# Optimization experiments

Measured on AMD Instinct MI355X. Metric: run time of the kernel, lower is better.

## Reference

```python
import jax, jax.numpy as jnp
import numpy as np

N_NODES = 100000
N_GRAPHS = 256
N_EDGES = 800000


def gcn_conv(x, W, b, src, dst):
    """PyG GCNConv: self-loops + symmetric deg^-1/2 normalization + scatter-add."""
    h = x @ W  # [N, F_out]
    # degree on graph with self-loops (edge weight 1)
    deg = jax.ops.segment_sum(jnp.ones((src.shape[0],), h.dtype), dst,
                              num_segments=N_NODES) + 1.0
    dinv = jax.lax.rsqrt(deg)  # deg^-1/2, deg >= 1 so finite
    norm = dinv[src] * dinv[dst]  # [E]
    msg = h[src] * norm[:, None]  # gather + scale, [E, F_out]
    agg = jax.ops.segment_sum(msg, dst, num_segments=N_NODES)
    # self-loop contribution: dinv[i]^2 * h[i]
    agg = agg + h * (dinv * dinv)[:, None]
    return agg + b


def setup_inputs() -> dict:
    key = jax.random.key(0)
    ks = jax.random.split(key, 16)
    inp = {
        "x": jax.random.normal(ks[0], (N_NODES, 114), jnp.float32),
        "edge_index": jax.random.randint(ks[1], (2, N_EDGES), 0, N_NODES, jnp.int64)
        if jax.config.jax_enable_x64 else jax.random.randint(ks[1], (2, N_EDGES), 0, N_NODES, jnp.int32),
        "batch": jnp.sort(jax.random.randint(ks[2], (N_NODES,), 0, N_GRAPHS,
                                             jnp.int32)),
        "W1": jax.random.normal(ks[3], (114, 230), jnp.float32) * 0.09,
        "b1": jax.random.normal(ks[4], (230,), jnp.float32) * 0.01,
        "W2": jax.random.normal(ks[5], (230, 115), jnp.float32) * 0.07,
        "b2": jax.random.normal(ks[6], (115,), jnp.float32) * 0.01,
        "Wg": jax.random.normal(ks[7], (115, 64), jnp.float32) * 0.09,
        "bg": jax.random.normal(ks[8], (64,), jnp.float32) * 0.01,
        "Wf": jax.random.normal(ks[9], (64, 32), jnp.float32) * 0.12,
        "bf": jax.random.normal(ks[10], (32,), jnp.float32) * 0.01,
        "Wo": jax.random.normal(ks[11], (32, 1), jnp.float32) * 0.17,
        "bo": jax.random.normal(ks[12], (1,), jnp.float32) * 0.01,
    }
    return inp


def reference(x, edge_index, batch, W1, b1, W2, b2, Wg, bg, Wf, bf, Wo, bo):
    src, dst = edge_index[0], edge_index[1]
    h = jax.nn.relu(gcn_conv(x, W1, b1, src, dst))
    # dropout p=0.2 is identity at inference (training=False)
    h = jax.nn.relu(gcn_conv(h, W2, b2, src, dst))
    # global max pool over graphs; h >= 0 after relu so clamp empty segments to 0
    pooled = jax.ops.segment_max(h, batch, num_segments=N_GRAPHS)
    pooled = jnp.maximum(pooled, 0.0)  # [G, 115]
    g = jax.nn.relu(pooled @ Wg + bg)
    g = jax.nn.relu(g @ Wf + bf)
    return g @ Wo + bo  # [G, 1]
```

## Files before the change

### kernel.cpp

```cpp
#include <hip/hip_runtime.h>
#include <hip/hip_bf16.h>
#include <hip/hip_fp16.h>

#define NN 100000
#define NG 256
#define NE 800000

constexpr int F0 = 114;
constexpr int F1 = 230;
constexpr int F2 = 115;
constexpr int MPAD = 100096;

typedef _Float16 __attribute__((ext_vector_type(8))) f16x8;
typedef __attribute__((ext_vector_type(4))) float f32x4;
typedef __attribute__((ext_vector_type(8))) unsigned short u16x8;

__device__ __forceinline__ unsigned short f2h_bits(float x) {
  _Float16 h = (_Float16)x;
  return __builtin_bit_cast(unsigned short, h);
}
__device__ __forceinline__ float h_bits2f(unsigned short u) {
  return (float)__builtin_bit_cast(_Float16, u);
}

__device__ __forceinline__ void bar_nodrain() {
  asm volatile("s_waitcnt lgkmcnt(0)" ::: "memory");
  __builtin_amdgcn_s_barrier();
}


__global__ void k_count(const int* __restrict__ dst, int* __restrict__ cnt) {
  int e = blockIdx.x * blockDim.x + threadIdx.x;
  if (e < NE) atomicAdd(&cnt[dst[e]], 1);
}

constexpr int SCAN_T = 256;
constexpr int SCAN_E = 1024;
constexpr int NB = (NN + SCAN_E - 1) / SCAN_E;

__global__ void k_scan1(const int* __restrict__ cnt, int* __restrict__ off,
                        int* __restrict__ bsum, float* __restrict__ dinv) {
  __shared__ int s[SCAN_T];
  int b = blockIdx.x, t = threadIdx.x;
  int base = b * SCAN_E + t * 4;
  int v0 = 0, v1 = 0, v2 = 0, v3 = 0;
  if (base + 0 < NN) v0 = cnt[base + 0];
  if (base + 1 < NN) v1 = cnt[base + 1];
  if (base + 2 < NN) v2 = cnt[base + 2];
  if (base + 3 < NN) v3 = cnt[base + 3];
  if (base + 0 < NN) dinv[base + 0] = rsqrtf((float)v0 + 1.0f);
  if (base + 1 < NN) dinv[base + 1] = rsqrtf((float)v1 + 1.0f);
  if (base + 2 < NN) dinv[base + 2] = rsqrtf((float)v2 + 1.0f);
  if (base + 3 < NN) dinv[base + 3] = rsqrtf((float)v3 + 1.0f);
  int sum = v0 + v1 + v2 + v3;
  s[t] = sum;
  __syncthreads();
  for (int ofs = 1; ofs < SCAN_T; ofs <<= 1) {
    int x = (t >= ofs) ? s[t - ofs] : 0;
    __syncthreads();
    s[t] += x;
    __syncthreads();
  }
  int excl = s[t] - sum;
  if (base + 0 < NN) off[base + 0] = excl;
  if (base + 1 < NN) off[base + 1] = excl + v0;
  if (base + 2 < NN) off[base + 2] = excl + v0 + v1;
  if (base + 3 < NN) off[base + 3] = excl + v0 + v1 + v2;
  if (t == SCAN_T - 1) bsum[b] = s[t];
}

__global__ void k_scan3(int* __restrict__ off, const int* __restrict__ bsum,
                        int* __restrict__ cur) {
  __shared__ int pre;
  int b = blockIdx.x, t = threadIdx.x;
  int seg = b >> 2;
  if (t < 64) {
    int s = 0;
    for (int j = t; j < seg; j += 64) s += bsum[j];
#pragma unroll
    for (int o = 1; o < 64; o <<= 1) s += __shfl_xor(s, o);
    if (t == 0) pre = s;
  }
  __syncthreads();
  int i = b * 256 + t;
  if (i < NN) {
    int v = off[i] + pre;
    off[i] = v;
    cur[i] = v;
  }
  if (i == NN) off[NN] = NE;
}


constexpr int FB_PLACE = (NE + 255) / 256;
constexpr int FB_PREPX = NN / 2;
constexpr int FB_PREPB = 256;
constexpr int FB_POOL  = (NG * F2 + 255) / 256;

__global__ __launch_bounds__(256) void k_fatB(
    const int* __restrict__ src, const int* __restrict__ dst,
    int* __restrict__ cur, int* __restrict__ srcs,
    const float* __restrict__ x, const float* __restrict__ dinv,
    unsigned short* __restrict__ xd,
    const float* __restrict__ W1, const float* __restrict__ W2,
    unsigned short* __restrict__ B1, unsigned short* __restrict__ B2,
    float* __restrict__ pooled) {
  int b = blockIdx.x, t = threadIdx.x;
  if (b < FB_PLACE) {
    int e = b * 256 + t;
    if (e < NE) {
      int p = atomicAdd(&cur[dst[e]], 1);
      srcs[p] = src[e];
    }
  } else if (b < FB_PLACE + FB_PREPX) {
    int bb = b - FB_PLACE;
    int n = bb * 2 + (t >> 7);
    int f = t & 127;
    float v = (f < F0) ? x[(size_t)n * F0 + f] * dinv[n] : 0.0f;
    xd[(size_t)n * 128 + f] = f2h_bits(v);
  } else if (b < FB_PLACE + FB_PREPX + FB_PREPB) {
    int bb = b - (FB_PLACE + FB_PREPX);
    if (bb < 128) {
      int n = bb * 2 + (t >> 7), k = t & 127;
      float v = (k < F0 && n < F1) ? W1[(size_t)k * F1 + n] : 0.0f;
      B1[(size_t)n * 128 + k] = f2h_bits(v);
    } else {
      int n = bb - 128, k = t;
      float v = (k < F1 && n < F2) ? W2[(size_t)k * F2 + n] : 0.0f;
      B2[(size_t)n * 256 + k] = f2h_bits(v);
    }
  } else {
    int bb = b - (FB_PLACE + FB_PREPX + FB_PREPB);
    int i = bb * 256 + t;
    if (i < NG * F2) pooled[i] = 0.0f;
  }
}


template <bool POOL>
__global__ __launch_bounds__(256) void k_gatherw(
    const unsigned short* __restrict__ tab, const float* __restrict__ dinv,
    const int* __restrict__ off, const int* __restrict__ srcs,
    const float* __restrict__ b2, const int* __restrict__ batch,
    unsigned short* __restrict__ outh, float* __restrict__ pooled) {
  __shared__ float smax[4][128];
  __shared__ int sg[4];
  int w = threadIdx.x >> 6, lane = threadIdx.x & 63;
  int n = blockIdx.x * 4 + w;
  int grp = lane >> 4, sub = lane & 15;
  int fb = sub * 8;

  float acc[8] = {0.f, 0.f, 0.f, 0.f, 0.f, 0.f, 0.f, 0.f};
  int j0 = off[n], j1 = off[n + 1];
  for (int base = j0; base <= j1; base += 16) {
    int row[4];
    u16x8 v[4];
    bool has[4];
#pragma unroll
    for (int c = 0; c < 4; ++c) {
      int je = base + c * 4 + grp;
      row[c] = (je < j1) ? srcs[je] : ((je == j1) ? n : -1);
      has[c] = row[c] >= 0;
    }
#pragma unroll
    for (int c = 0; c < 4; ++c)
      if (has[c]) v[c] = *(const u16x8*)&tab[(size_t)row[c] * 128 + fb];
#pragma unroll
    for (int c = 0; c < 4; ++c)
      if (has[c]) {
#pragma unroll
        for (int u = 0; u < 8; ++u) acc[u] += h_bits2f(v[c][u]);
      }
  }
#pragma unroll
  for (int u = 0; u < 8; ++u) {
    acc[u] += __shfl_xor(acc[u], 16);
    acc[u] += __shfl_xor(acc[u], 32);
  }
  float dn = dinv[n];

  if constexpr (!POOL) {
    if (grp == 0) {
      u16x8 o;
#pragma unroll
      for (int u = 0; u < 8; ++u) o[u] = f2h_bits(acc[u] * dn);
      *(u16x8*)&outh[(size_t)n * 128 + fb] = o;
    }
  } else {
    if (grp == 0) {
#pragma unroll
      for (int u = 0; u < 8; ++u) {
        int f = fb + u;
        float bb = (f < F2) ? b2[f] : 0.0f;
        smax[w][f] = fmaxf(acc[u] * dn + bb, 0.0f);
      }
      if (sub == 0) sg[w] = batch[n];
    }
    __syncthreads();
    int t = threadIdx.x;
    if (t < 128) {
      int g0 = sg[0];
      bool same = (sg[1] == g0) & (sg[2] == g0) & (sg[3] == g0);
      if (same) {
        float m = fmaxf(fmaxf(smax[0][t], smax[1][t]),
                        fmaxf(smax[2][t], smax[3][t]));
        if (t < F2 && m > 0.0f)
          atomicMax((int*)&pooled[g0 * F2 + t], __float_as_int(m));
      } else {
        for (int ww = 0; ww < 4; ++ww) {
          float m = smax[ww][t];
          if (t < F2 && m > 0.0f)
            atomicMax((int*)&pooled[sg[ww] * F2 + t], __float_as_int(m));
        }
      }
    }
  }
}


__global__ __launch_bounds__(256, 3) void k_fused(
    const unsigned short* __restrict__ A,
    const unsigned short* __restrict__ B1,
    const unsigned short* __restrict__ B2,
    const float* __restrict__ b1, const float* __restrict__ dscale,
    unsigned short* __restrict__ td) {
  __shared__ char lds[49152];
  char* AsB = lds;
  char* h1B = lds + 16384;
  char* Bs  = lds + 32768;

  const int t = threadIdx.x;
  const int m0 = blockIdx.x * 64;
  const int lane = t & 63, w = t >> 6;
  const int r = lane & 15;
  const int kq = lane >> 4;
  const int kb16 = kq * 16;
  const int rq = kq * 4;
  const int wc = w * 32;
  const int swr = (r & 7) << 4;
  const int arow = t >> 2, aseg = t & 3, aswz = (arow & 7) << 4;
  const int brow = t >> 1, bseg = t & 1, bswz = (brow & 7) << 4;

  {
    size_t ga = (size_t)(m0 + arow) * 128 + aseg * 32;
#pragma unroll
    for (int v = 0; v < 4; ++v) {
      u16x8 d = *(const u16x8*)&A[ga + v * 8];
      *(u16x8*)(AsB + arow * 256 + ((aseg * 64 + v * 16) ^ aswz)) = d;
    }
  }
  u16x8 ph[4];
  {
    size_t gb = (size_t)brow * 128 + bseg * 32;
#pragma unroll
    for (int v = 0; v < 4; ++v) ph[v] = *(const u16x8*)&B1[gb + v * 8];
  }

  f32x4 acc1[4][2], acc2[4][2];
#pragma unroll
  for (int i = 0; i < 4; ++i)
#pragma unroll
    for (int j = 0; j < 2; ++j) {
      acc1[i][j] = (f32x4){0.f, 0.f, 0.f, 0.f};
      acc2[i][j] = (f32x4){0.f, 0.f, 0.f, 0.f};
    }

#pragma unroll
  for (int rd = 0; rd < 8; ++rd) {
    const int h = rd >> 2, phase = (rd >> 1) & 1, kc = rd & 1;
    bar_nodrain();
#pragma unroll
    for (int v = 0; v < 4; ++v)
      *(u16x8*)(Bs + brow * 128 + ((bseg * 64 + v * 16) ^ bswz)) = ph[v];
    if (rd < 7) {
      const int nr = rd + 1, nh = nr >> 2, nph = (nr >> 1) & 1, nkc = nr & 1;
      const unsigned short* G = (nph == 0) ? B1 : B2;
      const size_t gb = (nph == 0)
          ? (size_t)(nh * 128 + brow) * 128 + nkc * 64 + bseg * 32
          : (size_t)brow * 256 + nh * 128 + nkc * 64 + bseg * 32;
#pragma unroll
      for (int v = 0; v < 4; ++v) ph[v] = *(const u16x8*)&G[gb + v * 8];
    }
    bar_nodrain();

    if (phase == 0) {
#pragma unroll
      for (int ks = 0; ks < 2; ++ks) {
        f16x8 av[4], bv[2];
#pragma unroll
        for (int i = 0; i < 4; ++i)
          av[i] = *(const f16x8*)(AsB + (i * 16 + r) * 256 +
                                  ((kc * 128 + ks * 64 + kb16) ^ swr));
#pragma unroll
        for (int j = 0; j < 2; ++j)
          bv[j] = *(const f16x8*)(Bs + (wc + j * 16 + r) * 128 +
                                  ((ks * 64 + kb16) ^ swr));
#pragma unroll
        for (int i = 0; i < 4; ++i)
#pragma unroll
          for (int j = 0; j < 2; ++j)
            acc1[i][j] = __builtin_amdgcn_mfma_f32_16x16x32_f16(av[i], bv[j], acc1[i][j], 0, 0, 0);
      }
      if (kc == 1) {
#pragma unroll
        for (int i = 0; i < 4; ++i)
#pragma unroll
          for (int j = 0; j < 2; ++j) {
            const int nl = wc + j * 16 + r;
            const int n = h * 128 + nl;
            const bool val = n < F1;
            const float bb = val ? b1[n] : 0.0f;
#pragma unroll
            for (int q = 0; q < 4; ++q) {
              const int ml = i * 16 + rq + q;
              const float v = val ? fmaxf(acc1[i][j][q] + bb, 0.0f) : 0.0f;
              *(unsigned short*)(h1B + ml * 256 + ((nl * 2) ^ ((ml & 7) << 4))) = f2h_bits(v);
            }
          }
#pragma unroll
        for (int i = 0; i < 4; ++i)
#pragma unroll
          for (int j = 0; j < 2; ++j) acc1[i][j] = (f32x4){0.f, 0.f, 0.f, 0.f};
      }
    } else {
#pragma unroll
      for (int ks = 0; ks < 2; ++ks) {
        f16x8 ah[4], bv[2];
#pragma unroll
        for (int i = 0; i < 4; ++i) {
          const int row = i * 16 + r;
          ah[i] = *(const f16x8*)(h1B + row * 256 +
                                  ((kc * 128 + ks * 64 + kb16) ^ swr));
        }
#pragma unroll
        for (int j = 0; j < 2; ++j)
          bv[j] = *(const f16x8*)(Bs + (wc + j * 16 + r) * 128 +
                                  ((ks * 64 + kb16) ^ swr));
#pragma unroll
        for (int i = 0; i < 4; ++i)
#pragma unroll
          for (int j = 0; j < 2; ++j)
            acc2[i][j] = __builtin_amdgcn_mfma_f32_16x16x32_f16(ah[i], bv[j], acc2[i][j], 0, 0, 0);
      }
    }
  }

  __syncthreads();
#pragma unroll
  for (int i = 0; i < 4; ++i)
#pragma unroll
    for (int j = 0; j < 2; ++j) {
      const int nl = wc + j * 16 + r;
#pragma unroll
      for (int q = 0; q < 4; ++q) {
        const int ml = i * 16 + rq + q;
        const float v = acc2[i][j][q] * dscale[m0 + ml];
        *(unsigned short*)(h1B + ml * 256 + ((nl * 2) ^ ((ml & 7) << 4))) = f2h_bits(v);
      }
    }
  __syncthreads();
  {
    const int row = t >> 2, seg = t & 3;
    const int swz = (row & 7) << 4;
    const size_t dst = (size_t)(m0 + row) * 128 + seg * 32;
#pragma unroll
    for (int v = 0; v < 4; ++v) {
      u16x8 d = *(const u16x8*)(h1B + row * 256 + ((seg * 64 + v * 16) ^ swz));
      *(u16x8*)&td[dst + v * 8] = d;
    }
  }
}


__global__ void k_mlp(const float* __restrict__ pooled,
                      const float* __restrict__ Wg, const float* __restrict__ bg,
                      const float* __restrict__ Wf, const float* __restrict__ bf,
                      const float* __restrict__ Wo, const float* __restrict__ bo,
                      float* __restrict__ out) {
  __shared__ float sp[F2];
  __shared__ float sg[64];
  __shared__ float sf[32];
  int g = blockIdx.x, t = threadIdx.x;
  for (int f = t; f < F2; f += 64) sp[f] = pooled[g * F2 + f];
  __syncthreads();
  float a = bg[t];
  for (int k = 0; k < F2; ++k) a += sp[k] * Wg[k * 64 + t];
  sg[t] = fmaxf(a, 0.0f);
  __syncthreads();
  if (t < 32) {
    float c = bf[t];
    for (int k = 0; k < 64; ++k) c += sg[k] * Wf[k * 32 + t];
    sf[t] = fmaxf(c, 0.0f);
  }
  __syncthreads();
  if (t == 0) {
    float c = bo[0];
    for (int k = 0; k < 32; ++k) c += sf[k] * Wo[k];
    out[g] = c;
  }
}


extern "C" void kernel_launch(void* const* d_in, const int* in_sizes, int n_in,
                              void* d_out, int out_size, void* d_ws, size_t ws_size,
                              hipStream_t stream) {
  const float* x  = (const float*)d_in[0];
  const int* ei   = (const int*)d_in[1];
  const int* batch = (const int*)d_in[2];
  const float* W1 = (const float*)d_in[3];
  const float* b1 = (const float*)d_in[4];
  const float* W2 = (const float*)d_in[5];
  const float* b2 = (const float*)d_in[6];
  const float* Wg = (const float*)d_in[7];
  const float* bg = (const float*)d_in[8];
  const float* Wf = (const float*)d_in[9];
  const float* bf = (const float*)d_in[10];
  const float* Wo = (const float*)d_in[11];
  const float* bo = (const float*)d_in[12];
  const int* src = ei;
  const int* dst = ei + NE;

  char* p = (char*)d_ws;
  auto alloc4 = [&](size_t units) { void* r = p; p += units * 4; return r; };
  float* dinv  = (float*)alloc4(100224);
  int* cnt     = (int*)alloc4(100224);
  int* off     = (int*)alloc4(100352);
  int* cur     = (int*)alloc4(100224);
  int* bsum    = (int*)alloc4(128);
  int* srcs    = (int*)alloc4(NE);
  unsigned short* xd   = (unsigned short*)alloc4((size_t)NN * 128 / 2);
  unsigned short* aggX = (unsigned short*)alloc4((size_t)MPAD * 128 / 2);
  unsigned short* td   = (unsigned short*)alloc4((size_t)MPAD * 128 / 2);
  unsigned short* Bt1  = (unsigned short*)alloc4(256 * 128 / 2);
  unsigned short* Bt2  = (unsigned short*)alloc4(128 * 256 / 2);
  float* pooled = (float*)alloc4((size_t)NG * F2);

  hipMemsetAsync(cnt, 0, 100224 * sizeof(int), stream);

  k_count<<<(NE + 255) / 256, 256, 0, stream>>>(dst, cnt);
  k_scan1<<<NB, SCAN_T, 0, stream>>>(cnt, off, bsum, dinv);
  k_scan3<<<(NN + 256) / 256, 256, 0, stream>>>(off, bsum, cur);

  k_fatB<<<FB_PLACE + FB_PREPX + FB_PREPB + FB_POOL, 256, 0, stream>>>(
      src, dst, cur, srcs, x, dinv, xd, W1, W2, Bt1, Bt2, pooled);

  k_gatherw<false><<<NN / 4, 256, 0, stream>>>(xd, dinv, off, srcs,
                                               nullptr, nullptr, aggX, nullptr);

  k_fused<<<MPAD / 64, 256, 0, stream>>>(aggX, Bt1, Bt2, b1, dinv, td);

  k_gatherw<true><<<NN / 4, 256, 0, stream>>>(td, dinv, off, srcs,
                                              b2, batch, nullptr, pooled);

  k_mlp<<<NG, 64, 0, stream>>>(pooled, Wg, bg, Wf, bf, Wo, bo, (float*)d_out);
}
```

Measured before the change: 272.0 us.

## Slice feature tables into 16-column panels for cache-local gathers

Stores the fp16 node feature tables (xd and td) as eight column slices of 16 features each, so each slice is about 3.2 MB. The aggregation kernels now run blocks per slice (blockIdx & 7), with two threads per node walking its edges, so random row gathers touch a much smaller working set that should stay in L2/MALL. The pooled max is now reduced per block in LDS slots keyed by graph id before the global atomicMax. In exchange, the CSR offsets and source indices are re-read eight times per pass, and per-thread edge loops become serial with more divergence across uneven node degrees.

```diff
diff --git a/kernel.cpp b/kernel.cpp
--- a/kernel.cpp
+++ b/kernel.cpp
@@ -93,7 +93,7 @@
 
 
 constexpr int FB_PLACE = (NE + 255) / 256;
-constexpr int FB_PREPX = NN / 2;
+constexpr int FB_PREPX = MPAD / 16;
 constexpr int FB_PREPB = 256;
 constexpr int FB_POOL  = (NG * F2 + 255) / 256;
 
@@ -114,10 +114,18 @@
     }
   } else if (b < FB_PLACE + FB_PREPX) {
     int bb = b - FB_PLACE;
-    int n = bb * 2 + (t >> 7);
-    int f = t & 127;
-    float v = (f < F0) ? x[(size_t)n * F0 + f] * dinv[n] : 0.0f;
-    xd[(size_t)n * 128 + f] = f2h_bits(v);
+    int n = bb * 16 + (t >> 4);
+    int c = t & 15;
+    int s = c >> 1, pp = c & 1;
+    float dn = (n < NN) ? dinv[n] : 0.0f;
+    u16x8 o;
+#pragma unroll
+    for (int u = 0; u < 8; ++u) {
+      int f = c * 8 + u;
+      float v = (n < NN && f < F0) ? x[(size_t)n * F0 + f] * dn : 0.0f;
+      o[u] = f2h_bits(v);
+    }
+    *(u16x8*)&xd[((size_t)s * MPAD + n) * 16 + pp * 8] = o;
   } else if (b < FB_PLACE + FB_PREPX + FB_PREPB) {
     int bb = b - (FB_PLACE + FB_PREPX);
     if (bb < 128) {
@@ -138,81 +146,86 @@
 
 
 template <bool POOL>
-__global__ __launch_bounds__(256) void k_gatherw(
-    const unsigned short* __restrict__ tab, const float* __restrict__ dinv,
+__global__ __launch_bounds__(256) void k_gslice(
+    const unsigned short* __restrict__ tab,
+    const float* __restrict__ dinv,
     const int* __restrict__ off, const int* __restrict__ srcs,
     const float* __restrict__ b2, const int* __restrict__ batch,
-    unsigned short* __restrict__ outh, float* __restrict__ pooled) {
-  __shared__ float smax[4][128];
-  __shared__ int sg[4];
-  int w = threadIdx.x >> 6, lane = threadIdx.x & 63;
-  int n = blockIdx.x * 4 + w;
-  int grp = lane >> 4, sub = lane & 15;
-  int fb = sub * 8;
+    unsigned short* __restrict__ aggX, float* __restrict__ pooled) {
+  __shared__ int lmax[4][16];
+  __shared__ int g0s;
+  const int s = blockIdx.x & 7;
+  const int nb = blockIdx.x >> 3;
+  const int t = threadIdx.x;
+  const int n = nb * 128 + (t >> 1);
+  const int p = t & 1;
+  const unsigned short* slice = tab + (size_t)s * MPAD * 16;
+
+  if (POOL) {
+    if (t < 64) lmax[t >> 4][t & 15] = 0;
+    if (t == 0) g0s = batch[nb * 128];
+    __syncthreads();
+  }
 
   float acc[8] = {0.f, 0.f, 0.f, 0.f, 0.f, 0.f, 0.f, 0.f};
-  int j0 = off[n], j1 = off[n + 1];
-  for (int base = j0; base <= j1; base += 16) {
-    int row[4];
-    u16x8 v[4];
-    bool has[4];
-#pragma unroll
-    for (int c = 0; c < 4; ++c) {
-      int je = base + c * 4 + grp;
-      row[c] = (je < j1) ? srcs[je] : ((je == j1) ? n : -1);
-      has[c] = row[c] >= 0;
-    }
-#pragma unroll
-    for (int c = 0; c < 4; ++c)
-      if (has[c]) v[c] = *(const u16x8*)&tab[(size_t)row[c] * 128 + fb];
-#pragma unroll
-    for (int c = 0; c < 4; ++c)
-      if (has[c]) {
-#pragma unroll
-        for (int u = 0; u < 8; ++u) acc[u] += h_bits2f(v[c][u]);
-      }
-  }
-#pragma unroll
-  for (int u = 0; u < 8; ++u) {
-    acc[u] += __shfl_xor(acc[u], 16);
-    acc[u] += __shfl_xor(acc[u], 32);
-  }
-  float dn = dinv[n];
-
-  if constexpr (!POOL) {
-    if (grp == 0) {
+  const bool valid = n < NN;
+  if (valid) {
+    int j0 = __builtin_nontemporal_load(&off[n]);
+    int j1 = __builtin_nontemporal_load(&off[n + 1]);
+    for (int j = j0; j <= j1; j += 4) {
+      int row[4];
+      u16x8 v[4];
+      bool has[4];
+#pragma unroll
+      for (int c = 0; c < 4; ++c) {
+        int je = j + c;
+        row[c] = (je < j1) ? __builtin_nontemporal_load(&srcs[je])
+                           : ((je == j1) ? n : -1);
+        has[c] = row[c] >= 0;
+      }
+#pragma unroll
+      for (int c = 0; c < 4; ++c)
+        if (has[c]) v[c] = *(const u16x8*)&slice[(size_t)row[c] * 16 + p * 8];
+#pragma unroll
+      for (int c = 0; c < 4; ++c)
+        if (has[c]) {
+#pragma unroll
+          for (int u = 0; u < 8; ++u) acc[u] += h_bits2f(v[c][u]);
+        }
+    }
+    float dn = dinv[n];
+    if constexpr (!POOL) {
       u16x8 o;
 #pragma unroll
       for (int u = 0; u < 8; ++u) o[u] = f2h_bits(acc[u] * dn);
-      *(u16x8*)&outh[(size_t)n * 128 + fb] = o;
-    }
-  } else {
-    if (grp == 0) {
+      __builtin_nontemporal_store(o, (u16x8*)&aggX[(size_t)n * 128 + s * 16 + p * 8]);
+    } else {
+      int g = batch[n];
+      int slot = g - g0s;
 #pragma unroll
       for (int u = 0; u < 8; ++u) {
-        int f = fb + u;
-        float bb = (f < F2) ? b2[f] : 0.0f;
-        smax[w][f] = fmaxf(acc[u] * dn + bb, 0.0f);
-      }
-      if (sub == 0) sg[w] = batch[n];
-    }
+        int col = s * 16 + p * 8 + u;
+        if (col < F2) {
+          float v = fmaxf(acc[u] * dn + b2[col], 0.0f);
+          if (v > 0.0f) {
+            if (slot >= 0 && slot < 4)
+              atomicMax(&lmax[slot][p * 8 + u], __float_as_int(v));
+            else
+              atomicMax((int*)&pooled[g * F2 + col], __float_as_int(v));
+          }
+        }
+      }
+    }
+  }
+  if (POOL) {
     __syncthreads();
-    int t = threadIdx.x;
-    if (t < 128) {
-      int g0 = sg[0];
-      bool same = (sg[1] == g0) & (sg[2] == g0) & (sg[3] == g0);
-      if (same) {
-        float m = fmaxf(fmaxf(smax[0][t], smax[1][t]),
-                        fmaxf(smax[2][t], smax[3][t]));
-        if (t < F2 && m > 0.0f)
-          atomicMax((int*)&pooled[g0 * F2 + t], __float_as_int(m));
-      } else {
-        for (int ww = 0; ww < 4; ++ww) {
-          float m = smax[ww][t];
-          if (t < F2 && m > 0.0f)
-            atomicMax((int*)&pooled[sg[ww] * F2 + t], __float_as_int(m));
-        }
-      }
+    if (t < 64) {
+      int slot = t >> 4, c16 = t & 15;
+      int m = lmax[slot][c16];
+      int col = s * 16 + c16;
+      int g = g0s + slot;
+      if (m > 0 && col < F2 && g < NG)
+        atomicMax((int*)&pooled[g * F2 + col], m);
     }
   }
 }
@@ -360,13 +373,14 @@
     }
   __syncthreads();
   {
-    const int row = t >> 2, seg = t & 3;
+    const int row = t >> 2, q = t & 3;
     const int swz = (row & 7) << 4;
-    const size_t dst = (size_t)(m0 + row) * 128 + seg * 32;
-#pragma unroll
-    for (int v = 0; v < 4; ++v) {
-      u16x8 d = *(const u16x8*)(h1B + row * 256 + ((seg * 64 + v * 16) ^ swz));
-      *(u16x8*)&td[dst + v * 8] = d;
+#pragma unroll
+    for (int e = 0; e < 2; ++e) {
+      const int s = q * 2 + e;
+      const size_t base = ((size_t)s * MPAD + m0 + row) * 16;
+      *(u16x8*)&td[base]     = *(const u16x8*)(h1B + row * 256 + ((s * 32) ^ swz));
+      *(u16x8*)&td[base + 8] = *(const u16x8*)(h1B + row * 256 + ((s * 32 + 16) ^ swz));
     }
   }
 }
@@ -428,9 +442,9 @@
   int* cur     = (int*)alloc4(100224);
   int* bsum    = (int*)alloc4(128);
   int* srcs    = (int*)alloc4(NE);
-  unsigned short* xd   = (unsigned short*)alloc4((size_t)NN * 128 / 2);
+  unsigned short* xd   = (unsigned short*)alloc4((size_t)8 * MPAD * 16 / 2);
   unsigned short* aggX = (unsigned short*)alloc4((size_t)MPAD * 128 / 2);
-  unsigned short* td   = (unsigned short*)alloc4((size_t)MPAD * 128 / 2);
+  unsigned short* td   = (unsigned short*)alloc4((size_t)8 * MPAD * 16 / 2);
   unsigned short* Bt1  = (unsigned short*)alloc4(256 * 128 / 2);
   unsigned short* Bt2  = (unsigned short*)alloc4(128 * 256 / 2);
   float* pooled = (float*)alloc4((size_t)NG * F2);
@@ -444,13 +458,13 @@
   k_fatB<<<FB_PLACE + FB_PREPX + FB_PREPB + FB_POOL, 256, 0, stream>>>(
       src, dst, cur, srcs, x, dinv, xd, W1, W2, Bt1, Bt2, pooled);
 
-  k_gatherw<false><<<NN / 4, 256, 0, stream>>>(xd, dinv, off, srcs,
-                                               nullptr, nullptr, aggX, nullptr);
+  k_gslice<false><<<8 * (MPAD / 128), 256, 0, stream>>>(
+      xd, dinv, off, srcs, nullptr, nullptr, aggX, nullptr);
 
   k_fused<<<MPAD / 64, 256, 0, stream>>>(aggX, Bt1, Bt2, b1, dinv, td);
 
-  k_gatherw<true><<<NN / 4, 256, 0, stream>>>(td, dinv, off, srcs,
-                                              b2, batch, nullptr, pooled);
+  k_gslice<true><<<8 * (MPAD / 128), 256, 0, stream>>>(
+      td, dinv, off, srcs, b2, batch, nullptr, pooled);
 
   k_mlp<<<NG, 64, 0, stream>>>(pooled, Wg, bg, Wf, bf, Wo, bo, (float*)d_out);
 }
```

Result: slower. 328.9 us (+20.9%).
